# Kernel tuning notes

Hardware: AMD Instinct MI355X
Metric: run time of the kernel (lower is better)

The kernel has to match this reference:

```python
import jax, jax.numpy as jnp
import numpy as np

B, S, H, DH, E = 8, 2048, 1024, 4096, 8
ALPHA = 0.5
LN_EPS = 1e-5


def setup_inputs() -> dict:
    key = jax.random.key(0)
    ks = jax.random.split(key, 8)
    sc = 0.02
    return {
        "x": jax.random.normal(ks[0], (B, S, H), jnp.float32),
        "We1": jax.random.normal(ks[1], (E, H, DH), jnp.float32) * sc,
        "be1": jnp.zeros((E, DH), jnp.float32),
        "We2": jax.random.normal(ks[2], (E, DH, H), jnp.float32) * sc,
        "be2": jnp.zeros((E, H), jnp.float32),
        "Wq": jax.random.normal(ks[3], (H, H), jnp.float32) * sc,
        "bq": jnp.zeros((H,), jnp.float32),
        "Wk": jax.random.normal(ks[4], (H, H), jnp.float32) * sc,
        "bk": jnp.zeros((H,), jnp.float32),
        "Wv": jax.random.normal(ks[5], (H, H), jnp.float32) * sc,
        "bv": jnp.zeros((H,), jnp.float32),
        "ln_g": jnp.ones((H,), jnp.float32),
        "ln_b": jnp.zeros((H,), jnp.float32),
        "current_expert_idx": E - 1,
    }


def _boosting_forward(x, We1, be1, We2, be2, Wq, bq, Wk, bk, Wv, bv, ln_g, ln_b, cur):
    sg = jax.lax.stop_gradient
    n = cur + 1  # static Python int: number of experts executed
    boost = sg(x)  # boost_input = x.detach()
    outs = []
    for i in range(n):
        h = jax.nn.relu(jnp.einsum("bsh,hf->bsf", boost, We1[i]) + be1[i])
        eo = jnp.einsum("bsf,fh->bsh", h, We2[i]) + be2[i]  # dropout = identity (eval)
        if i < n - 1:
            eo = sg(eo)  # earlier experts detached
        boost = boost + ALPHA * eo
        outs.append(eo)
    stacked = jnp.stack(outs, axis=2)  # [B,S,n,H]
    q = jnp.einsum("bsh,hd->bsd", x, Wq) + bq          # [B,S,H]
    k = jnp.einsum("bseh,hd->bsed", stacked, Wk) + bk  # [B,S,n,H]
    v = jnp.einsum("bseh,hd->bsed", stacked, Wv) + bv
    scores = jnp.einsum("bsd,bsed->bse", q, k) / jnp.sqrt(jnp.asarray(H, x.dtype))
    w = jax.nn.softmax(scores, axis=-1)                # [B,S,n]
    fused = jnp.einsum("bse,bsed->bsd", w, v)          # [B,S,H]
    y = x + fused
    mu = jnp.mean(y, axis=-1, keepdims=True)
    var = jnp.mean(jnp.square(y - mu), axis=-1, keepdims=True)
    return (y - mu) * jax.lax.rsqrt(var + LN_EPS) * ln_g + ln_b


def reference(x, We1, be1, We2, be2, Wq, bq, Wk, bk, Wv, bv, ln_g, ln_b, current_expert_idx):
    return _boosting_forward(x, We1, be1, We2, be2, Wq, bq, Wk, bk, Wv, bv, ln_g, ln_b, int(current_expert_idx))
```

## Files before the change

### kernel.cpp

```cpp
#include <hip/hip_runtime.h>
#include <math.h>

typedef __bf16 bf16_t;
typedef __bf16 bf16x8 __attribute__((ext_vector_type(8)));
typedef __bf16 bf16x4 __attribute__((ext_vector_type(4)));
typedef float f32x4 __attribute__((ext_vector_type(4)));
typedef unsigned int u32;

static constexpr int kBd = 8, kS = 2048, kH = 1024, kDH = 4096, kE = 8;
static constexpr int kM = kBd * kS;
static constexpr float kScale = 0.03125f;

__device__ __forceinline__ void gload_lds16(const void* g, void* l) {
  __builtin_amdgcn_global_load_lds(
      (const __attribute__((address_space(1))) u32*)g,
      (__attribute__((address_space(3))) u32*)l, 16, 0, 0);
}

__global__ __launch_bounds__(256) void cvt_flat_kernel(const float* __restrict__ in,
                                                       bf16_t* __restrict__ out, int n4) {
  int i = blockIdx.x * 256 + threadIdx.x;
  if (i >= n4) return;
  f32x4 v = *(const f32x4*)(in + (size_t)i * 4);
  bf16x4 o;
#pragma unroll
  for (int j = 0; j < 4; ++j) o[j] = (bf16_t)v[j];
  *(bf16x4*)(out + (size_t)i * 4) = o;
}

__global__ __launch_bounds__(256) void transpose_cvt_kernel(
    const float* __restrict__ in, bf16_t* __restrict__ out, int R, int C) {
  __shared__ float tile[32][33];
  int tx = threadIdx.x & 31, ty = threadIdx.x >> 5;
  int c0 = blockIdx.x * 32, r0 = blockIdx.y * 32;
#pragma unroll
  for (int yy = 0; yy < 4; ++yy)
    tile[ty + yy * 8][tx] = in[(size_t)(r0 + ty + yy * 8) * C + c0 + tx];
  __syncthreads();
#pragma unroll
  for (int yy = 0; yy < 4; ++yy)
    out[(size_t)(c0 + ty + yy * 8) * R + r0 + tx] = (bf16_t)tile[tx][ty + yy * 8];
}

template <int MODE>
__global__ __launch_bounds__(512, 2) void gemm256_kernel(
    const bf16_t* __restrict__ A, const bf16_t* __restrict__ Bt,
    int M, int N, int K, int nwg,
    const float* __restrict__ bias,
    bf16_t* __restrict__ outb,
    const float* __restrict__ bin_f, float* __restrict__ bout_f,
    const bf16_t* __restrict__ bin_b, bf16_t* __restrict__ bout_b,
    bf16_t* __restrict__ stacked,
    const float* __restrict__ xres, float* __restrict__ yout,
    const int* __restrict__ curp, int expert_i) {
  if ((MODE == 0 || MODE == 1 || MODE == 4) && expert_i > *curp) return;
  extern __shared__ char lds_buf[];
  char* Abase = lds_buf;
  char* Bbase = lds_buf + 65536;
  const int tid = threadIdx.x;
  const int lane = tid & 63, wid = tid >> 6;
  const int wr = wid >> 2, wc = wid & 3;
  const int fr = lane & 15, fh = lane >> 4;
  const int lane_swz = (fr * 64 + fh * 16) ^ ((fr >> 3) << 5);
  const int bid = blockIdx.x;
  const int wg = (bid & 7) * (nwg >> 3) + (bid >> 3);
  const int nMb = M >> 8;
  const int m0 = (wg % nMb) << 8, n0 = (wg / nMb) << 8;
  int grow[2], gcol[2];
#pragma unroll
  for (int j = 0; j < 2; ++j) {
    int L = (j * 512 + tid) * 16;
    int Lp = L ^ (((L >> 9) & 1) << 5);
    int s = Lp >> 10;
    grow[j] = ((s >> 1) << 4) + ((Lp >> 6) & 15);
    gcol[j] = ((s & 1) << 5) + (((Lp >> 4) & 3) << 3);
  }
  const bf16_t* sA[2] = {A + (size_t)(m0 + grow[0]) * K + gcol[0],
                         A + (size_t)(m0 + grow[1]) * K + gcol[1]};
  const bf16_t* sB[2] = {Bt + (size_t)(n0 + grow[0]) * K + gcol[0],
                         Bt + (size_t)(n0 + grow[1]) * K + gcol[1]};
  const size_t rstep = (size_t)128 * K;

#define STAGE(SP, BASE, tau, h)                                               \
  {                                                                           \
    char* d_ = (BASE) + ((h) << 14) + (wid << 10);                            \
    gload_lds16(SP[0] + (size_t)(h)*rstep + (size_t)(tau)*64, d_);            \
    gload_lds16(SP[1] + (size_t)(h)*rstep + (size_t)(tau)*64, d_ + 8192);     \
  }
#define STAGE_A(t, h) STAGE(sA, Abase + (((t)&1) << 15), (t), (h))
#define STAGE_B(t, h) STAGE(sB, Bbase + (((t)&1) << 15), (t), (h))

  const int bq = (wc & 1) * 4;

  f32x4 acc[8][4] = {};
  bf16x8 b[4][2];
  bf16x8 a0_, a1_, a2_, a3_;
  const int NT = K >> 6;

#define PHASE(q, PAR, STG, G)                                                  \
  {                                                                            \
    if ((q) == 0) {                                                            \
      const char* Br = Bbase + (PAR)*32768 + ((wc >> 1) << 14) + lane_swz;     \
      _Pragma("unroll") for (int nf = 0; nf < 4; ++nf)                         \
          _Pragma("unroll") for (int kk = 0; kk < 2; ++kk)                     \
          b[nf][kk] = *(const bf16x8*)(Br + ((bq + nf) * 2 + kk) * 1024);      \
    }                                                                          \
    {                                                                          \
      const char* Ar = Abase + (PAR)*32768 + (wr << 14) + lane_swz;            \
      a0_ = *(const bf16x8*)(Ar + ((2 * (q)) * 2 + 0) * 1024);                 \
      a1_ = *(const bf16x8*)(Ar + ((2 * (q)) * 2 + 1) * 1024);                 \
      a2_ = *(const bf16x8*)(Ar + ((2 * (q) + 1) * 2 + 0) * 1024);             \
      a3_ = *(const bf16x8*)(Ar + ((2 * (q) + 1) * 2 + 1) * 1024);             \
    }                                                                          \
    STG;                                                                       \
    if ((q) == 0) asm volatile("s_waitcnt lgkmcnt(8)" ::: "memory");           \
    __builtin_amdgcn_s_barrier();                                              \
    asm volatile("s_waitcnt lgkmcnt(0)" ::: "memory");                         \
    __builtin_amdgcn_sched_barrier(0);                                         \
    __builtin_amdgcn_s_setprio(1);                                             \
    _Pragma("unroll") for (int nf = 0; nf < 4; ++nf) {                         \
      acc[2 * (q)][nf] = __builtin_amdgcn_mfma_f32_16x16x32_bf16(              \
          a0_, b[nf][0], acc[2 * (q)][nf], 0, 0, 0);                           \
      acc[2 * (q)][nf] = __builtin_amdgcn_mfma_f32_16x16x32_bf16(              \
          a1_, b[nf][1], acc[2 * (q)][nf], 0, 0, 0);                           \
      acc[2 * (q) + 1][nf] = __builtin_amdgcn_mfma_f32_16x16x32_bf16(          \
          a2_, b[nf][0], acc[2 * (q) + 1][nf], 0, 0, 0);                       \
      acc[2 * (q) + 1][nf] = __builtin_amdgcn_mfma_f32_16x16x32_bf16(          \
          a3_, b[nf][1], acc[2 * (q) + 1][nf], 0, 0, 0);                       \
    }                                                                          \
    __builtin_amdgcn_s_setprio(0);                                             \
    if ((G) == 1) {                                                            \
      if (last)                                                                \
        asm volatile("s_waitcnt vmcnt(0)" ::: "memory");                       \
      else                                                                     \
        asm volatile("s_waitcnt vmcnt(4)" ::: "memory");                       \
    }                                                                          \
    __builtin_amdgcn_s_barrier();                                              \
  }

  STAGE_A(0, 0); STAGE_A(0, 1);
  STAGE_B(0, 0); STAGE_B(0, 1);
  STAGE_B(1, 0); STAGE_B(1, 1);
  asm volatile("s_waitcnt vmcnt(4)" ::: "memory");
  __builtin_amdgcn_s_barrier();

  const int nit = NT >> 1;
  for (int j = 0; j < nit; ++j) {
    const int t1 = 2 * j + 1, t2 = 2 * j + 2, t3 = 2 * j + 3;
    const bool last = (j == nit - 1);
    PHASE(0, 0, STAGE_A(t1, 0), 0);
    PHASE(1, 0, STAGE_A(t1, 1), 0);
    PHASE(2, 0, if (t2 < NT) STAGE_B(t2, 0), 0);
    PHASE(3, 0, if (t2 < NT) STAGE_B(t2, 1), 1);
    PHASE(0, 1, if (t2 < NT) STAGE_A(t2, 0), 0);
    PHASE(1, 1, if (t2 < NT) STAGE_A(t2, 1), 0);
    PHASE(2, 1, if (t3 < NT) STAGE_B(t3, 0), 0);
    PHASE(3, 1, if (t3 < NT) STAGE_B(t3, 1), 1);
  }
#undef PHASE
#undef STAGE
#undef STAGE_A
#undef STAGE_B

#pragma unroll
  for (int nf = 0; nf < 4; ++nf) {
    const int col = n0 + wc * 64 + nf * 16 + fr;
    const float bv = bias ? bias[col] : 0.0f;
#pragma unroll
    for (int mf = 0; mf < 8; ++mf) {
#pragma unroll
      for (int r = 0; r < 4; ++r) {
        const int row = m0 + wr * 128 + mf * 16 + fh * 4 + r;
        const size_t idx = (size_t)row * N + col;
        float v = acc[mf][nf][r] + bv;
        if (MODE == 0) {
          outb[idx] = (bf16_t)(v > 0.0f ? v : 0.0f);
        } else if (MODE == 2) {
          outb[idx] = (bf16_t)v;
        } else if (MODE == 1) {
          float nb2 = bin_f[idx] + 0.5f * v;
          bout_f[idx] = nb2;
          bout_b[idx] = (bf16_t)nb2;
          stacked[idx] = (bf16_t)v;
        } else if (MODE == 4) {
          float nb2 = (float)bin_b[idx] + 0.5f * v;
          bout_b[idx] = (bf16_t)nb2;
          stacked[idx] = (bf16_t)v;
        } else {
          yout[idx] = v + xres[idx];
        }
      }
    }
  }
}

__global__ __launch_bounds__(256) void scores_mix_kernel(
    const bf16_t* __restrict__ qk, const bf16_t* __restrict__ q,
    const float* __restrict__ bk, const bf16_t* __restrict__ stacked,
    bf16_t* __restrict__ mix, const int* __restrict__ curp) {
  const int n = *curp + 1;
  int lane = threadIdx.x & 63, wave = threadIdx.x >> 6;
  int m = blockIdx.x * 4 + wave;
  size_t base = (size_t)m * kH + lane * 16;
  int c0 = lane * 16;
  bf16x8 qk0 = *(const bf16x8*)(qk + base);
  bf16x8 qk1 = *(const bf16x8*)(qk + base + 8);
  bf16x8 q0 = *(const bf16x8*)(q + base);
  bf16x8 q1 = *(const bf16x8*)(q + base + 8);
  float sc[kE + 1];
  bf16x8 eo0[kE], eo1[kE];
#pragma unroll
  for (int e = 0; e < kE; ++e) {
    sc[e] = 0.0f;
    if (e < n) {
      size_t sb = (size_t)e * kM * kH + base;
      eo0[e] = *(const bf16x8*)(stacked + sb);
      eo1[e] = *(const bf16x8*)(stacked + sb + 8);
      float d = 0.0f;
#pragma unroll
      for (int j = 0; j < 8; ++j)
        d += (float)eo0[e][j] * (float)qk0[j] + (float)eo1[e][j] * (float)qk1[j];
      sc[e] = d;
    }
  }
  {
    float qb = 0.0f;
#pragma unroll
    for (int j = 0; j < 8; ++j)
      qb += (float)q0[j] * bk[c0 + j] + (float)q1[j] * bk[c0 + 8 + j];
    sc[kE] = qb;
  }
#pragma unroll
  for (int off = 32; off >= 1; off >>= 1)
#pragma unroll
    for (int e = 0; e <= kE; ++e) sc[e] += __shfl_xor(sc[e], off, 64);
  float s[kE];
  float mx = -1e30f;
#pragma unroll
  for (int e = 0; e < kE; ++e)
    if (e < n) {
      s[e] = (sc[e] + sc[kE]) * kScale;
      mx = fmaxf(mx, s[e]);
    }
  float Z = 0.0f;
#pragma unroll
  for (int e = 0; e < kE; ++e)
    if (e < n) {
      s[e] = expf(s[e] - mx);
      Z += s[e];
    }
  float inv = 1.0f / Z;
  float mv[16];
#pragma unroll
  for (int j = 0; j < 16; ++j) mv[j] = 0.0f;
#pragma unroll
  for (int e = 0; e < kE; ++e)
    if (e < n) {
      float w = s[e] * inv;
#pragma unroll
      for (int j = 0; j < 8; ++j) {
        mv[j] += w * (float)eo0[e][j];
        mv[8 + j] += w * (float)eo1[e][j];
      }
    }
  bf16x8 o0, o1;
#pragma unroll
  for (int j = 0; j < 8; ++j) {
    o0[j] = (bf16_t)mv[j];
    o1[j] = (bf16_t)mv[8 + j];
  }
  *(bf16x8*)(mix + base) = o0;
  *(bf16x8*)(mix + base + 8) = o1;
}

__global__ __launch_bounds__(256) void layernorm_kernel(
    const float* __restrict__ y, const float* __restrict__ g,
    const float* __restrict__ b, float* __restrict__ out) {
  int lane = threadIdx.x & 63, wave = threadIdx.x >> 6;
  int m = blockIdx.x * 4 + wave;
  size_t base = (size_t)m * kH + lane * 16;
  f32x4 v[4];
#pragma unroll
  for (int j = 0; j < 4; ++j) v[j] = *(const f32x4*)(y + base + j * 4);
  float s = 0.0f, s2 = 0.0f;
#pragma unroll
  for (int j = 0; j < 4; ++j)
#pragma unroll
    for (int t = 0; t < 4; ++t) {
      float u = v[j][t];
      s += u;
      s2 += u * u;
    }
#pragma unroll
  for (int off = 32; off >= 1; off >>= 1) {
    s += __shfl_xor(s, off, 64);
    s2 += __shfl_xor(s2, off, 64);
  }
  float mu = s * (1.0f / kH);
  float var = s2 * (1.0f / kH) - mu * mu;
  float rs = rsqrtf(var + 1e-5f);
  int c0 = lane * 16;
#pragma unroll
  for (int j = 0; j < 4; ++j) {
    f32x4 gg = *(const f32x4*)(g + c0 + j * 4);
    f32x4 bb = *(const f32x4*)(b + c0 + j * 4);
    f32x4 o;
#pragma unroll
    for (int t = 0; t < 4; ++t) o[t] = (v[j][t] - mu) * rs * gg[t] + bb[t];
    *(f32x4*)(out + base + j * 4) = o;
  }
}

extern "C" void kernel_launch(void* const* d_in, const int* in_sizes, int n_in,
                              void* d_out, int out_size, void* d_ws, size_t ws_size,
                              hipStream_t stream) {
  const float* x = (const float*)d_in[0];
  const float* We1 = (const float*)d_in[1];
  const float* be1 = (const float*)d_in[2];
  const float* We2 = (const float*)d_in[3];
  const float* be2 = (const float*)d_in[4];
  const float* Wq = (const float*)d_in[5];
  const float* bq = (const float*)d_in[6];
  const float* Wk = (const float*)d_in[7];
  const float* bk = (const float*)d_in[8];
  const float* Wv = (const float*)d_in[9];
  const float* bv = (const float*)d_in[10];
  const float* ln_g = (const float*)d_in[11];
  const float* ln_b = (const float*)d_in[12];
  const int* curp = (const int*)d_in[13];
  float* out = (float*)d_out;

  char* ws = (char*)d_ws;
  const size_t MB = 1ull << 20;
  bf16_t* stacked = (bf16_t*)(ws);
  bf16_t* xb = (bf16_t*)(ws + 256 * MB);
  bf16_t* boostb = (bf16_t*)(ws + 288 * MB);
  bf16_t* wA = (bf16_t*)(ws + 320 * MB);
  bf16_t* wB = (bf16_t*)(ws + 328 * MB);
  bf16_t* WqT = (bf16_t*)(ws + 336 * MB);
  bf16_t* WkC = (bf16_t*)(ws + 338 * MB);
  bf16_t* WvT = (bf16_t*)(ws + 340 * MB);
  char* dyn = ws + 342 * MB;
  size_t rem = ws_size > 342 * MB ? ws_size - 342 * MB : 0;
  int nchunk;
  bool f32boost;
  if (rem >= 192 * MB) { nchunk = 1; f32boost = true; }
  else if (rem >= 128 * MB) { nchunk = 1; f32boost = false; }
  else if (rem >= 64 * MB) { nchunk = 2; f32boost = false; }
  else { nchunk = 4; f32boost = false; }
  bf16_t* hbuf = (bf16_t*)dyn;
  float* boostf = (float*)(dyn + 128 * MB);
  bf16_t* qb_ = hbuf;
  bf16_t* qkb = boostb;
  bf16_t* mixb = xb;
  float* yf = (float*)ws;

  const int Mc = kM / nchunk;
  const size_t MH = (size_t)kM * kH;
  const u32 kLds = 131072;
  dim3 blk(256), blk5(512);

  cvt_flat_kernel<<<(kM * kH) / 1024, blk, 0, stream>>>(x, xb, (kM * kH) / 4);
  cvt_flat_kernel<<<(kH * kH) / 1024, blk, 0, stream>>>(Wk, WkC, (kH * kH) / 4);
  transpose_cvt_kernel<<<dim3(kH / 32, kH / 32), blk, 0, stream>>>(Wq, WqT, kH, kH);
  transpose_cvt_kernel<<<dim3(kH / 32, kH / 32), blk, 0, stream>>>(Wv, WvT, kH, kH);

  for (int i = 0; i < kE; ++i) {
    transpose_cvt_kernel<<<dim3(kDH / 32, kH / 32), blk, 0, stream>>>(
        We1 + (size_t)i * kH * kDH, wA, kH, kDH);
    transpose_cvt_kernel<<<dim3(kH / 32, kDH / 32), blk, 0, stream>>>(
        We2 + (size_t)i * kH * kDH, wB, kDH, kH);
    for (int c = 0; c < nchunk; ++c) {
      const size_t ro = (size_t)c * Mc * kH;
      const bf16_t* Ain = ((i == 0) ? xb : boostb) + ro;
      {
        int nwg = (Mc / 256) * (kDH / 256);
        gemm256_kernel<0><<<nwg, blk5, kLds, stream>>>(
            Ain, wA, Mc, kDH, kH, nwg, be1 + (size_t)i * kDH, hbuf,
            nullptr, nullptr, nullptr, nullptr, nullptr, nullptr, nullptr, curp, i);
      }
      int nwg = (Mc / 256) * (kH / 256);
      if (f32boost) {
        const float* bin = ((i == 0) ? x : boostf) + ro;
        gemm256_kernel<1><<<nwg, blk5, kLds, stream>>>(
            hbuf, wB, Mc, kH, kDH, nwg, be2 + (size_t)i * kH, nullptr,
            bin, boostf + ro, nullptr, boostb + ro, stacked + (size_t)i * MH + ro,
            nullptr, nullptr, curp, i);
      } else {
        const bf16_t* binb = ((i == 0) ? xb : boostb) + ro;
        gemm256_kernel<4><<<nwg, blk5, kLds, stream>>>(
            hbuf, wB, Mc, kH, kDH, nwg, be2 + (size_t)i * kH, nullptr,
            nullptr, nullptr, binb, boostb + ro, stacked + (size_t)i * MH + ro,
            nullptr, nullptr, curp, i);
      }
    }
  }

  const int nwgH = (kM / 256) * (kH / 256);
  gemm256_kernel<2><<<nwgH, blk5, kLds, stream>>>(
      xb, WqT, kM, kH, kH, nwgH, bq, qb_,
      nullptr, nullptr, nullptr, nullptr, nullptr, nullptr, nullptr, curp, 0);
  gemm256_kernel<2><<<nwgH, blk5, kLds, stream>>>(
      qb_, WkC, kM, kH, kH, nwgH, nullptr, qkb,
      nullptr, nullptr, nullptr, nullptr, nullptr, nullptr, nullptr, curp, 0);
  scores_mix_kernel<<<dim3(kM / 4), blk, 0, stream>>>(qkb, qb_, bk, stacked, mixb, curp);
  gemm256_kernel<3><<<nwgH, blk5, kLds, stream>>>(
      mixb, WvT, kM, kH, kH, nwgH, bv, nullptr,
      nullptr, nullptr, nullptr, nullptr, nullptr, x, yf, curp, 0);
  layernorm_kernel<<<dim3(kM / 4), blk, 0, stream>>>(yf, ln_g, ln_b, out);
}
```

Baseline: 3.082 ms.

## Triple-buffer A tiles in LDS to prefetch two k-steps ahead

The GEMM kernel now keeps three rotating LDS buffers for the A operand instead of two. A tiles are loaded two k-iterations ahead, with the global-to-LDS wait relaxed from vmcnt(4) to vmcnt(8) to match. Dynamic LDS grows from 128 KB to 160 KB. The aim is to hide more global-load latency behind the MFMA work, at the cost of using the full per-CU LDS and slightly more address bookkeeping.

```diff
diff --git a/kernel.cpp b/kernel.cpp
--- a/kernel.cpp
+++ b/kernel.cpp
@@ -56,7 +56,7 @@
   if ((MODE == 0 || MODE == 1 || MODE == 4) && expert_i > *curp) return;
   extern __shared__ char lds_buf[];
   char* Abase = lds_buf;
-  char* Bbase = lds_buf + 65536;
+  char* Bbase = lds_buf + 98304;
   const int tid = threadIdx.x;
   const int lane = tid & 63, wid = tid >> 6;
   const int wr = wid >> 2, wc = wid & 3;
@@ -87,7 +87,7 @@
     gload_lds16(SP[0] + (size_t)(h)*rstep + (size_t)(tau)*64, d_);            \
     gload_lds16(SP[1] + (size_t)(h)*rstep + (size_t)(tau)*64, d_ + 8192);     \
   }
-#define STAGE_A(t, h) STAGE(sA, Abase + (((t)&1) << 15), (t), (h))
+#define STAGE_A(buf, t, h) STAGE(sA, Abase + (buf)*32768, (t), (h))
 #define STAGE_B(t, h) STAGE(sB, Bbase + (((t)&1) << 15), (t), (h))
 
   const int bq = (wc & 1) * 4;
@@ -97,7 +97,7 @@
   bf16x8 a0_, a1_, a2_, a3_;
   const int NT = K >> 6;
 
-#define PHASE(q, PAR, STG, G)                                                  \
+#define PHASE(q, ABUF, PAR, STG, G)                                            \
   {                                                                            \
     if ((q) == 0) {                                                            \
       const char* Br = Bbase + (PAR)*32768 + ((wc >> 1) << 14) + lane_swz;     \
@@ -106,7 +106,7 @@
           b[nf][kk] = *(const bf16x8*)(Br + ((bq + nf) * 2 + kk) * 1024);      \
     }                                                                          \
     {                                                                          \
-      const char* Ar = Abase + (PAR)*32768 + (wr << 14) + lane_swz;            \
+      const char* Ar = Abase + (ABUF)*32768 + (wr << 14) + lane_swz;           \
       a0_ = *(const bf16x8*)(Ar + ((2 * (q)) * 2 + 0) * 1024);                 \
       a1_ = *(const bf16x8*)(Ar + ((2 * (q)) * 2 + 1) * 1024);                 \
       a2_ = *(const bf16x8*)(Ar + ((2 * (q) + 1) * 2 + 0) * 1024);             \
@@ -133,29 +133,34 @@
       if (last)                                                                \
         asm volatile("s_waitcnt vmcnt(0)" ::: "memory");                       \
       else                                                                     \
-        asm volatile("s_waitcnt vmcnt(4)" ::: "memory");                       \
+        asm volatile("s_waitcnt vmcnt(8)" ::: "memory");                       \
     }                                                                          \
     __builtin_amdgcn_s_barrier();                                              \
   }
 
-  STAGE_A(0, 0); STAGE_A(0, 1);
+  STAGE_A(0, 0, 0); STAGE_A(0, 0, 1);
   STAGE_B(0, 0); STAGE_B(0, 1);
+  STAGE_A(1, 1, 0); STAGE_A(1, 1, 1);
   STAGE_B(1, 0); STAGE_B(1, 1);
-  asm volatile("s_waitcnt vmcnt(4)" ::: "memory");
+  asm volatile("s_waitcnt vmcnt(8)" ::: "memory");
   __builtin_amdgcn_s_barrier();
 
   const int nit = NT >> 1;
+  int am0 = 0;
   for (int j = 0; j < nit; ++j) {
-    const int t1 = 2 * j + 1, t2 = 2 * j + 2, t3 = 2 * j + 3;
+    const int t2 = 2 * j + 2, t3 = 2 * j + 3;
     const bool last = (j == nit - 1);
-    PHASE(0, 0, STAGE_A(t1, 0), 0);
-    PHASE(1, 0, STAGE_A(t1, 1), 0);
-    PHASE(2, 0, if (t2 < NT) STAGE_B(t2, 0), 0);
-    PHASE(3, 0, if (t2 < NT) STAGE_B(t2, 1), 1);
-    PHASE(0, 1, if (t2 < NT) STAGE_A(t2, 0), 0);
-    PHASE(1, 1, if (t2 < NT) STAGE_A(t2, 1), 0);
-    PHASE(2, 1, if (t3 < NT) STAGE_B(t3, 0), 0);
-    PHASE(3, 1, if (t3 < NT) STAGE_B(t3, 1), 1);
+    int am1 = am0 + 1; if (am1 == 3) am1 = 0;
+    int am2 = am1 + 1; if (am2 == 3) am2 = 0;
+    PHASE(0, am0, 0, if (t2 < NT) STAGE_A(am2, t2, 0), 0);
+    PHASE(1, am0, 0, if (t2 < NT) STAGE_A(am2, t2, 1), 0);
+    PHASE(2, am0, 0, if (t2 < NT) STAGE_B(t2, 0), 0);
+    PHASE(3, am0, 0, if (t2 < NT) STAGE_B(t2, 1), 1);
+    PHASE(0, am1, 1, if (t3 < NT) STAGE_A(am0, t3, 0), 0);
+    PHASE(1, am1, 1, if (t3 < NT) STAGE_A(am0, t3, 1), 0);
+    PHASE(2, am1, 1, if (t3 < NT) STAGE_B(t3, 0), 0);
+    PHASE(3, am1, 1, if (t3 < NT) STAGE_B(t3, 1), 1);
+    am0 = am2;
   }
 #undef PHASE
 #undef STAGE
@@ -357,7 +362,7 @@
 
   const int Mc = kM / nchunk;
   const size_t MH = (size_t)kM * kH;
-  const u32 kLds = 131072;
+  const u32 kLds = 163840;
   dim3 blk(256), blk5(512);
 
   cvt_flat_kernel<<<(kM * kH) / 1024, blk, 0, stream>>>(x, xb, (kM * kH) / 4);
```

Result: no change. 3.107 ms (+0.8%).
